# Kernel optimization log

Hardware: AMD Instinct MI355X
Metric: run time of the kernel (lower is better)

Reference implementation:

```python
import jax, jax.numpy as jnp
import numpy as np

N_QUBITS = 8
INPUT_DIM = 256
SEQ_LEN = 256
BATCH = 512


def qgate(theta, x):
    # Closed-form expectation of the PennyLane circuit:
    #   RX(x_i) then RY(theta_i) on each wire (from |0>), then CNOT chain 0->1->...->n-1,
    #   measure <Z_k>.  Single-wire <Z_j> = cos(x_j) * cos(theta_j); CNOT chain maps
    #   Z_k -> Z_0 Z_1 ... Z_k in the Heisenberg picture, so on the product state
    #   <Z_k> = prod_{j<=k} cos(x_j) cos(theta_j).
    # x: (B, n_wires), theta: (n_wires,)
    return jnp.cumprod(jnp.cos(x) * jnp.cos(theta), axis=-1)


def setup_inputs() -> dict:
    key = jax.random.key(0)
    ks = jax.random.split(key, 14)
    d_in = INPUT_DIM + N_QUBITS  # concat([x, hx]) -> 264
    lin_scale = 1.0 / np.sqrt(d_in)
    inp = {
        "inputs": jax.random.normal(ks[0], (SEQ_LEN, BATCH, INPUT_DIM), dtype=jnp.float32),
        "Wf": jax.random.normal(ks[1], (N_QUBITS, d_in), dtype=jnp.float32) * lin_scale,
        "bf": jax.random.normal(ks[2], (N_QUBITS,), dtype=jnp.float32) * lin_scale,
        "Wi": jax.random.normal(ks[3], (N_QUBITS, d_in), dtype=jnp.float32) * lin_scale,
        "bi": jax.random.normal(ks[4], (N_QUBITS,), dtype=jnp.float32) * lin_scale,
        "Wu": jax.random.normal(ks[5], (N_QUBITS, d_in), dtype=jnp.float32) * lin_scale,
        "bu": jax.random.normal(ks[6], (N_QUBITS,), dtype=jnp.float32) * lin_scale,
        "Wo": jax.random.normal(ks[7], (N_QUBITS, d_in), dtype=jnp.float32) * lin_scale,
        "bo": jax.random.normal(ks[8], (N_QUBITS,), dtype=jnp.float32) * lin_scale,
        "pf": jax.random.normal(ks[9], (N_QUBITS,), dtype=jnp.float32),
        "pi_": jax.random.normal(ks[10], (N_QUBITS,), dtype=jnp.float32),
        "pu": jax.random.normal(ks[11], (N_QUBITS,), dtype=jnp.float32),
        "po": jax.random.normal(ks[12], (N_QUBITS,), dtype=jnp.float32),
    }
    return inp


def reference(inputs, Wf, bf, Wi, bi, Wu, bu, Wo, bo, pf, pi_, pu, po):
    B = inputs.shape[1]
    H = pf.shape[0]  # hidden_dim == n_qubits

    def step(carry, x):
        hx, cx = carry
        comb = jnp.concatenate([x, hx], axis=1)  # (B, input_dim + H)
        f = jax.nn.sigmoid(qgate(pf, comb @ Wf.T + bf))
        i = jax.nn.sigmoid(qgate(pi_, comb @ Wi.T + bi))
        g = jnp.tanh(qgate(pu, comb @ Wu.T + bu))
        o = jax.nn.sigmoid(qgate(po, comb @ Wo.T + bo))
        cx = f * cx + i * g
        hx = o * jnp.tanh(cx)
        return (hx, cx), hx

    init = (jnp.zeros((B, H), dtype=inputs.dtype), jnp.zeros((B, H), dtype=inputs.dtype))
    (hx, cx), stacked = jax.lax.scan(step, init, inputs)
    return stacked, hx, cx
```

## Files before the change

### kernel.cpp

```cpp
#include <hip/hip_runtime.h>
#include <hip/hip_bf16.h>


#define SEQ   256
#define BATCH 512
#define DIN   256
#define NROWS (SEQ * BATCH)
#define DCOMB 264
#define MCHUNKS 4

typedef __attribute__((ext_vector_type(8))) short short8;
typedef __attribute__((ext_vector_type(4))) float f32x4;
typedef __attribute__((ext_vector_type(2))) float f32x2;

__device__ __forceinline__ short f2bf(float f) {
    union { __hip_bfloat16 h; short s; } u;
    u.h = __float2bfloat16(f);
    return u.s;
}
__device__ __forceinline__ float bf2f(short s) {
    union { short s; __hip_bfloat16 h; } u;
    u.s = s;
    return __bfloat162float(u.h);
}

__device__ __forceinline__ short8 pack8(float4 a, float4 b) {
    union { short8 s8; int i[4]; } u;
    union { __hip_bfloat162 h; int i; } v;
    v.h = __float22bfloat162_rn(make_float2(a.x, a.y)); u.i[0] = v.i;
    v.h = __float22bfloat162_rn(make_float2(a.z, a.w)); u.i[1] = v.i;
    v.h = __float22bfloat162_rn(make_float2(b.x, b.y)); u.i[2] = v.i;
    v.h = __float22bfloat162_rn(make_float2(b.z, b.w)); u.i[3] = v.i;
    return u.s8;
}

__global__ __launch_bounds__(256) void qlstm_gemm(
    const float* __restrict__ X,
    const float* __restrict__ Wf, const float* __restrict__ Wi,
    const float* __restrict__ Wu, const float* __restrict__ Wo,
    const float* __restrict__ bfv, const float* __restrict__ biv,
    const float* __restrict__ buv, const float* __restrict__ bov,
    float* __restrict__ Z)
{
    const int l   = threadIdx.x & 63;
    const int wid = threadIdx.x >> 6;
    const int lm  = l & 15;
    const int lk  = l >> 4;

    const float* Wg[4] = {Wf, Wi, Wu, Wo};
    const float* Bg[4] = {bfv, biv, buv, bov};

    short8 Bhi[2][8], Blo[2][8];
    float bias[2];
    #pragma unroll
    for (int nt = 0; nt < 2; ++nt) {
        const int c = nt * 16 + lm;
        const float* wrow = Wg[c & 3] + (c >> 2) * DCOMB;
        bias[nt] = Bg[c & 3][c >> 2];
        #pragma unroll
        for (int ks = 0; ks < 8; ++ks) {
            const float* p = wrow + ks * 32 + lk * 8;
            const float4 w0 = *(const float4*)p;
            const float4 w1 = *(const float4*)(p + 4);
            const float wv[8] = {w0.x, w0.y, w0.z, w0.w, w1.x, w1.y, w1.z, w1.w};
            #pragma unroll
            for (int j = 0; j < 8; ++j) {
                const short hi = f2bf(wv[j]);
                Bhi[nt][ks][j] = hi;
                Blo[nt][ks][j] = f2bf(wv[j] - bf2f(hi));
            }
        }
    }

    #pragma unroll
    for (int ch = 0; ch < MCHUNKS; ++ch) {
        const int row0 = (blockIdx.x * MCHUNKS + ch) * 64 + wid * 16;
        const float* xbase = X + (long)(row0 + lm) * DIN + lk * 8;

        float4 xv[16];
        #pragma unroll
        for (int i = 0; i < 16; ++i)
            xv[i] = *(const float4*)(xbase + (i >> 1) * 32 + (i & 1) * 4);

        f32x4 acc0 = (f32x4){bias[0], bias[0], bias[0], bias[0]};
        f32x4 acc1 = (f32x4){bias[1], bias[1], bias[1], bias[1]};
        #pragma unroll
        for (int ks = 0; ks < 8; ++ks) {
            const short8 a = pack8(xv[2 * ks], xv[2 * ks + 1]);
            acc0 = __builtin_amdgcn_mfma_f32_16x16x32_bf16(a, Bhi[0][ks], acc0, 0, 0, 0);
            acc0 = __builtin_amdgcn_mfma_f32_16x16x32_bf16(a, Blo[0][ks], acc0, 0, 0, 0);
            acc1 = __builtin_amdgcn_mfma_f32_16x16x32_bf16(a, Bhi[1][ks], acc1, 0, 0, 0);
            acc1 = __builtin_amdgcn_mfma_f32_16x16x32_bf16(a, Blo[1][ks], acc1, 0, 0, 0);
        }

        #pragma unroll
        for (int r = 0; r < 4; ++r) {
            Z[(long)(row0 + lk * 4 + r) * 32 + lm]      = acc0[r];
            Z[(long)(row0 + lk * 4 + r) * 32 + 16 + lm] = acc1[r];
        }
    }
}

#define DPP_ROR(V, S) \
    __int_as_float(__builtin_amdgcn_update_dpp(__float_as_int(V), __float_as_int(V), 0x120 | (S), 0xF, 0xF, false))
#define SWAP8(V) \
    __int_as_float(__builtin_amdgcn_update_dpp(__float_as_int(V), __float_as_int(V), 0x128, 0xF, 0xF, false))
#define DPP_REPL8(V) \
    __int_as_float(__builtin_amdgcn_update_dpp(__float_as_int(V), __float_as_int(V), 0x118, 0xF, 0xF, false))

#define PSTG(A, D, PM) { \
    float s0_ = __int_as_float(__builtin_amdgcn_update_dpp(one_i, __float_as_int(A.x), 0x110 | (D), 0xF, 0xF, false)); \
    float s1_ = __int_as_float(__builtin_amdgcn_update_dpp(one_i, __float_as_int(A.y), 0x110 | (D), 0xF, 0xF, false)); \
    A *= (f32x2){ (PM) ? s0_ : 1.0f, (PM) ? s1_ : 1.0f }; }

#define PF 8

__global__ __launch_bounds__(64, 1) void qlstm_scan(
    const float* __restrict__ Z,
    const float* __restrict__ Wf, const float* __restrict__ Wi,
    const float* __restrict__ Wu, const float* __restrict__ Wo,
    const float* __restrict__ pf, const float* __restrict__ pi_,
    const float* __restrict__ pu, const float* __restrict__ po,
    float* __restrict__ out)
{
    const int tx  = threadIdx.x;
    const int q   = tx & 15;
    const int kq  = q & 7;
    const int hi  = q >> 3;
    const int b   = (blockIdx.x * 64 + tx) >> 4;
    const int oidx = b * 8 + kq;
    const int woff = kq * DCOMB + DIN;

    const float* WgA = hi ? Wu : Wf;
    const float* WgB = hi ? Wo : Wi;
    f32x2 wp[8];
    #pragma unroll
    for (int s = 0; s < 8; ++s) {
        const int j = (kq - s) & 7;
        wp[s] = (f32x2){WgA[woff + j], WgB[woff + j]};
    }
    const f32x2 cth = (f32x2){__cosf((hi ? pu : pf)[kq]),
                              __cosf((hi ? po : pi_)[kq])};

    const float SK1 = 0.25f, SK2 = -0.0208333333f, SK3 = 0.0020833333f,
                SK4 = -0.00021082f;
    const f32x2 k0 = (f32x2){hi ? 0.0f : 0.5f, 0.5f};
    const f32x2 k1 = (f32x2){hi ? 0.9999016f : SK1, SK1};
    const f32x2 k2 = (f32x2){hi ? -0.3310485f : SK2, SK2};
    const f32x2 k3 = (f32x2){hi ? 0.1204423f : SK3, SK3};
    const f32x2 k4 = (f32x2){hi ? -0.0277012f : SK4, SK4};

    const bool pm1 = kq >= 1, pm2 = kq >= 2, pm4 = kq >= 4;
    const int one_i = __float_as_int(1.0f);

    float hx = 0.0f, cx = 0.0f;
    const float2* __restrict__ Zv2 = (const float2*)Z;
    const int zoff = b * 16 + kq * 2 + hi;
    float* __restrict__ outp = out + oidx;

    float2 ring[PF];
    #pragma unroll
    for (int i = 0; i < PF; ++i) ring[i] = Zv2[(i << 13) + zoff];

    for (int t0 = 0; t0 < SEQ; t0 += PF) {
        #pragma unroll
        for (int u = 0; u < PF; ++u) {
            const int t = t0 + u;
            const float2 z2 = ring[u];
            int tn = t + PF; if (tn > SEQ - 1) tn = SEQ - 1;
            ring[u] = Zv2[(tn << 13) + zoff];

            const float h0 = hx;
            const float h1 = DPP_ROR(hx, 1), h2 = DPP_ROR(hx, 2);
            const float h3 = DPP_ROR(hx, 3), h4 = DPP_ROR(hx, 4);
            const float h5 = DPP_ROR(hx, 5), h6 = DPP_ROR(hx, 6);
            const float h7 = DPP_ROR(hx, 7);

            f32x2 ca = (f32x2){h0, h0} * wp[0] + (f32x2){h1, h1} * wp[1];
            f32x2 cb = (f32x2){h4, h4} * wp[4] + (f32x2){h5, h5} * wp[5];
            ca += (f32x2){h2, h2} * wp[2];
            cb += (f32x2){h6, h6} * wp[6];
            ca += (f32x2){h3, h3} * wp[3];
            cb += (f32x2){h7, h7} * wp[7];
            const f32x2 p = ((f32x2){z2.x, z2.y} + ca) + cb;

            f32x2 A = (f32x2){__cosf(p.x), __cosf(p.y)} * cth;
            PSTG(A, 1, pm1) PSTG(A, 2, pm2) PSTG(A, 4, pm4)

            const f32x2 t2 = A * A;
            f32x2 r = k3 + t2 * k4;
            r = k2 + t2 * r;
            r = k1 + t2 * r;
            const f32x2 P = k0 + A * r;
            const float v1 = P.x;
            const float v2 = P.y;

            const float swu = SWAP8(v1);
            cx = fmaf(v1, cx, v2 * swu);

            const float tq  = cx * cx;
            const float num = cx * fmaf(tq, fmaf(tq, 1.0f, 105.0f), 945.0f);
            const float den = fmaf(tq, fmaf(tq, 15.0f, 420.0f), 945.0f);
            const float tc  = num * __builtin_amdgcn_rcpf(den);

            const float stc = SWAP8(tc);
            const float hh  = v2 * stc;
            hx = SWAP8(hh);
            hx = DPP_REPL8(hx);

            outp[t << 12] = hx;
        }
    }
    if (q < 8) {
        out[NROWS * 8 + oidx]        = hx;
        out[NROWS * 8 + 4096 + oidx] = cx;
    }
}

extern "C" void kernel_launch(void* const* d_in, const int* in_sizes, int n_in,
                              void* d_out, int out_size, void* d_ws, size_t ws_size,
                              hipStream_t stream) {
    const float* X   = (const float*)d_in[0];
    const float* Wf  = (const float*)d_in[1];
    const float* bfv = (const float*)d_in[2];
    const float* Wi  = (const float*)d_in[3];
    const float* biv = (const float*)d_in[4];
    const float* Wu  = (const float*)d_in[5];
    const float* buv = (const float*)d_in[6];
    const float* Wo  = (const float*)d_in[7];
    const float* bov = (const float*)d_in[8];
    const float* pf  = (const float*)d_in[9];
    const float* pi_ = (const float*)d_in[10];
    const float* pu  = (const float*)d_in[11];
    const float* po  = (const float*)d_in[12];
    float* out = (float*)d_out;
    float* Z   = (float*)d_ws;

    qlstm_gemm<<<NROWS / (64 * MCHUNKS), 256, 0, stream>>>(
        X, Wf, Wi, Wu, Wo, bfv, biv, buv, bov, Z);
    qlstm_scan<<<128, 64, 0, stream>>>(Z, Wf, Wi, Wu, Wo, pf, pi_, pu, po, out);
}
```

Measured before the change: 264.8 us.

## Fuse projection GEMM and recurrent scan with flag-based producer-consumer overlap

```diff
diff --git a/kernel.cpp b/kernel.cpp
--- a/kernel.cpp
+++ b/kernel.cpp
@@ -7,7 +7,13 @@
 #define DIN   256
 #define NROWS (SEQ * BATCH)
 #define DCOMB 264
-#define MCHUNKS 4
+#define ZBYTES (NROWS * 32 * 4)
+
+#define NSCAN  32
+#define NBLK   512
+#define WSLOTS ((NBLK - NSCAN) * 4)
+#define NCHUNK (NROWS / 16)
+#define MAGIC  0x13579BDFu
 
 typedef __attribute__((ext_vector_type(8))) short short8;
 typedef __attribute__((ext_vector_type(4))) float f32x4;
@@ -23,7 +29,6 @@
     u.s = s;
     return __bfloat162float(u.h);
 }
-
 __device__ __forceinline__ short8 pack8(float4 a, float4 b) {
     union { short8 s8; int i[4]; } u;
     union { __hip_bfloat162 h; int i; } v;
@@ -34,80 +39,12 @@
     return u.s8;
 }
 
-__global__ __launch_bounds__(256) void qlstm_gemm(
-    const float* __restrict__ X,
-    const float* __restrict__ Wf, const float* __restrict__ Wi,
-    const float* __restrict__ Wu, const float* __restrict__ Wo,
-    const float* __restrict__ bfv, const float* __restrict__ biv,
-    const float* __restrict__ buv, const float* __restrict__ bov,
-    float* __restrict__ Z)
-{
-    const int l   = threadIdx.x & 63;
-    const int wid = threadIdx.x >> 6;
-    const int lm  = l & 15;
-    const int lk  = l >> 4;
-
-    const float* Wg[4] = {Wf, Wi, Wu, Wo};
-    const float* Bg[4] = {bfv, biv, buv, bov};
-
-    short8 Bhi[2][8], Blo[2][8];
-    float bias[2];
-    #pragma unroll
-    for (int nt = 0; nt < 2; ++nt) {
-        const int c = nt * 16 + lm;
-        const float* wrow = Wg[c & 3] + (c >> 2) * DCOMB;
-        bias[nt] = Bg[c & 3][c >> 2];
-        #pragma unroll
-        for (int ks = 0; ks < 8; ++ks) {
-            const float* p = wrow + ks * 32 + lk * 8;
-            const float4 w0 = *(const float4*)p;
-            const float4 w1 = *(const float4*)(p + 4);
-            const float wv[8] = {w0.x, w0.y, w0.z, w0.w, w1.x, w1.y, w1.z, w1.w};
-            #pragma unroll
-            for (int j = 0; j < 8; ++j) {
-                const short hi = f2bf(wv[j]);
-                Bhi[nt][ks][j] = hi;
-                Blo[nt][ks][j] = f2bf(wv[j] - bf2f(hi));
-            }
-        }
-    }
-
-    #pragma unroll
-    for (int ch = 0; ch < MCHUNKS; ++ch) {
-        const int row0 = (blockIdx.x * MCHUNKS + ch) * 64 + wid * 16;
-        const float* xbase = X + (long)(row0 + lm) * DIN + lk * 8;
-
-        float4 xv[16];
-        #pragma unroll
-        for (int i = 0; i < 16; ++i)
-            xv[i] = *(const float4*)(xbase + (i >> 1) * 32 + (i & 1) * 4);
-
-        f32x4 acc0 = (f32x4){bias[0], bias[0], bias[0], bias[0]};
-        f32x4 acc1 = (f32x4){bias[1], bias[1], bias[1], bias[1]};
-        #pragma unroll
-        for (int ks = 0; ks < 8; ++ks) {
-            const short8 a = pack8(xv[2 * ks], xv[2 * ks + 1]);
-            acc0 = __builtin_amdgcn_mfma_f32_16x16x32_bf16(a, Bhi[0][ks], acc0, 0, 0, 0);
-            acc0 = __builtin_amdgcn_mfma_f32_16x16x32_bf16(a, Blo[0][ks], acc0, 0, 0, 0);
-            acc1 = __builtin_amdgcn_mfma_f32_16x16x32_bf16(a, Bhi[1][ks], acc1, 0, 0, 0);
-            acc1 = __builtin_amdgcn_mfma_f32_16x16x32_bf16(a, Blo[1][ks], acc1, 0, 0, 0);
-        }
-
-        #pragma unroll
-        for (int r = 0; r < 4; ++r) {
-            Z[(long)(row0 + lk * 4 + r) * 32 + lm]      = acc0[r];
-            Z[(long)(row0 + lk * 4 + r) * 32 + 16 + lm] = acc1[r];
-        }
-    }
-}
-
 #define DPP_ROR(V, S) \
     __int_as_float(__builtin_amdgcn_update_dpp(__float_as_int(V), __float_as_int(V), 0x120 | (S), 0xF, 0xF, false))
 #define SWAP8(V) \
     __int_as_float(__builtin_amdgcn_update_dpp(__float_as_int(V), __float_as_int(V), 0x128, 0xF, 0xF, false))
 #define DPP_REPL8(V) \
     __int_as_float(__builtin_amdgcn_update_dpp(__float_as_int(V), __float_as_int(V), 0x118, 0xF, 0xF, false))
-
 #define PSTG(A, D, PM) { \
     float s0_ = __int_as_float(__builtin_amdgcn_update_dpp(one_i, __float_as_int(A.x), 0x110 | (D), 0xF, 0xF, false)); \
     float s1_ = __int_as_float(__builtin_amdgcn_update_dpp(one_i, __float_as_int(A.y), 0x110 | (D), 0xF, 0xF, false)); \
@@ -115,19 +52,91 @@
 
 #define PF 8
 
-__global__ __launch_bounds__(64, 1) void qlstm_scan(
-    const float* __restrict__ Z,
+__global__ __launch_bounds__(256) void flags_zero(unsigned* __restrict__ flags) {
+    flags[blockIdx.x * 256 + threadIdx.x] = 0u;
+}
+
+__global__ __launch_bounds__(256, 2) void qlstm_fused(
+    const float* __restrict__ X,
     const float* __restrict__ Wf, const float* __restrict__ Wi,
     const float* __restrict__ Wu, const float* __restrict__ Wo,
+    const float* __restrict__ bfv, const float* __restrict__ biv,
+    const float* __restrict__ buv, const float* __restrict__ bov,
     const float* __restrict__ pf, const float* __restrict__ pi_,
     const float* __restrict__ pu, const float* __restrict__ po,
+    float* __restrict__ Z, unsigned* __restrict__ flags,
     float* __restrict__ out)
 {
-    const int tx  = threadIdx.x;
-    const int q   = tx & 15;
-    const int kq  = q & 7;
-    const int hi  = q >> 3;
-    const int b   = (blockIdx.x * 64 + tx) >> 4;
+    const int wid = threadIdx.x >> 6;
+    const int l   = threadIdx.x & 63;
+
+    if (blockIdx.x >= NSCAN) {
+        const int lm = l & 15, lk = l >> 4;
+        const float* Wg[4] = {Wf, Wi, Wu, Wo};
+        const float* Bg[4] = {bfv, biv, buv, bov};
+
+        short8 Bhi[2][8], Blo[2][8];
+        float bias[2];
+        #pragma unroll
+        for (int nt = 0; nt < 2; ++nt) {
+            const int c = nt * 16 + lm;
+            const float* wrow = Wg[c & 3] + (c >> 2) * DCOMB;
+            bias[nt] = Bg[c & 3][c >> 2];
+            #pragma unroll
+            for (int ks = 0; ks < 8; ++ks) {
+                const float* p = wrow + ks * 32 + lk * 8;
+                const float4 w0 = *(const float4*)p;
+                const float4 w1 = *(const float4*)(p + 4);
+                const float wv[8] = {w0.x, w0.y, w0.z, w0.w, w1.x, w1.y, w1.z, w1.w};
+                #pragma unroll
+                for (int j = 0; j < 8; ++j) {
+                    const short hi = f2bf(wv[j]);
+                    Bhi[nt][ks][j] = hi;
+                    Blo[nt][ks][j] = f2bf(wv[j] - bf2f(hi));
+                }
+            }
+        }
+
+        const int wslot = (blockIdx.x - NSCAN) * 4 + wid;
+        #pragma unroll 1
+        for (int c = wslot; c < NCHUNK; c += WSLOTS) {
+            const int row0 = c * 16;
+            const float* xbase = X + (long)(row0 + lm) * DIN + lk * 8;
+
+            float4 xv[16];
+            #pragma unroll
+            for (int i = 0; i < 16; ++i)
+                xv[i] = *(const float4*)(xbase + (i >> 1) * 32 + (i & 1) * 4);
+
+            f32x4 acc0 = (f32x4){bias[0], bias[0], bias[0], bias[0]};
+            f32x4 acc1 = (f32x4){bias[1], bias[1], bias[1], bias[1]};
+            #pragma unroll
+            for (int ks = 0; ks < 8; ++ks) {
+                const short8 a = pack8(xv[2 * ks], xv[2 * ks + 1]);
+                acc0 = __builtin_amdgcn_mfma_f32_16x16x32_bf16(a, Bhi[0][ks], acc0, 0, 0, 0);
+                acc0 = __builtin_amdgcn_mfma_f32_16x16x32_bf16(a, Blo[0][ks], acc0, 0, 0, 0);
+                acc1 = __builtin_amdgcn_mfma_f32_16x16x32_bf16(a, Bhi[1][ks], acc1, 0, 0, 0);
+                acc1 = __builtin_amdgcn_mfma_f32_16x16x32_bf16(a, Blo[1][ks], acc1, 0, 0, 0);
+            }
+
+            #pragma unroll
+            for (int r = 0; r < 4; ++r) {
+                Z[(long)(row0 + lk * 4 + r) * 32 + lm]      = acc0[r];
+                Z[(long)(row0 + lk * 4 + r) * 32 + 16 + lm] = acc1[r];
+            }
+
+            if (l == 0)
+                __hip_atomic_store(&flags[c], MAGIC, __ATOMIC_RELEASE,
+                                   __HIP_MEMORY_SCOPE_AGENT);
+        }
+        return;
+    }
+
+    const int sid  = blockIdx.x * 256 + threadIdx.x;
+    const int q    = sid & 15;
+    const int kq   = q & 7;
+    const int hi   = q >> 3;
+    const int b    = sid >> 4;
     const int oidx = b * 8 + kq;
     const int woff = kq * DCOMB + DIN;
 
@@ -154,21 +163,49 @@
     const int one_i = __float_as_int(1.0f);
 
     float hx = 0.0f, cx = 0.0f;
-    const float2* __restrict__ Zv2 = (const float2*)Z;
     const int zoff = b * 16 + kq * 2 + hi;
     float* __restrict__ outp = out + oidx;
 
+    #define LDF(S, J) __hip_atomic_load( \
+        flags + ((S) * 32) + (l * 4 + (J)), __ATOMIC_RELAXED, __HIP_MEMORY_SCOPE_AGENT)
+    #define ZLD(SL) ({ \
+        union { unsigned long long u; float2 f; } cv_; \
+        cv_.u = __hip_atomic_load((const unsigned long long*)Z + \
+                 (((long)(SL)) << 13) + zoff, __ATOMIC_RELAXED, \
+                 __HIP_MEMORY_SCOPE_AGENT); \
+        cv_.f; })
+
+    #define SPIN8(S0) { \
+        for (int sp_ = 0; sp_ < (1 << 17); ++sp_) { \
+            unsigned a_ = LDF(S0, 0), b_ = LDF(S0, 1); \
+            unsigned c_ = LDF(S0, 2), d_ = LDF(S0, 3); \
+            if (__all((a_ == MAGIC) & (b_ == MAGIC) & (c_ == MAGIC) & (d_ == MAGIC))) break; \
+            __builtin_amdgcn_s_sleep(8); \
+        } }
+
+    SPIN8(0)
     float2 ring[PF];
     #pragma unroll
-    for (int i = 0; i < PF; ++i) ring[i] = Zv2[(i << 13) + zoff];
-
+    for (int i = 0; i < PF; ++i) ring[i] = ZLD(i);
+    unsigned f0 = LDF(PF, 0), f1 = LDF(PF, 1);
+    unsigned f2 = LDF(PF, 2), f3 = LDF(PF, 3);
+
+    #pragma unroll 1
     for (int t0 = 0; t0 < SEQ; t0 += PF) {
+        if (t0 + PF < SEQ) {
+            if (!__all((f0 == MAGIC) & (f1 == MAGIC) & (f2 == MAGIC) & (f3 == MAGIC)))
+                SPIN8(t0 + PF)
+            if (t0 + 2 * PF < SEQ) {
+                f0 = LDF(t0 + 2 * PF, 0); f1 = LDF(t0 + 2 * PF, 1);
+                f2 = LDF(t0 + 2 * PF, 2); f3 = LDF(t0 + 2 * PF, 3);
+            }
+        }
         #pragma unroll
         for (int u = 0; u < PF; ++u) {
             const int t = t0 + u;
             const float2 z2 = ring[u];
             int tn = t + PF; if (tn > SEQ - 1) tn = SEQ - 1;
-            ring[u] = Zv2[(tn << 13) + zoff];
+            ring[u] = ZLD(tn);
 
             const float h0 = hx;
             const float h1 = DPP_ROR(hx, 1), h2 = DPP_ROR(hx, 2);
@@ -234,9 +271,12 @@
     const float* pu  = (const float*)d_in[11];
     const float* po  = (const float*)d_in[12];
     float* out = (float*)d_out;
-    float* Z   = (float*)d_ws;
-
-    qlstm_gemm<<<NROWS / (64 * MCHUNKS), 256, 0, stream>>>(
-        X, Wf, Wi, Wu, Wo, bfv, biv, buv, bov, Z);
-    qlstm_scan<<<128, 64, 0, stream>>>(Z, Wf, Wi, Wu, Wo, pf, pi_, pu, po, out);
-}
+
+    char* ws = (char*)d_ws;
+    float*    Z     = (float*)ws;
+    unsigned* flags = (unsigned*)(ws + ZBYTES);
+
+    flags_zero<<<NCHUNK / 256, 256, 0, stream>>>(flags);
+    qlstm_fused<<<NBLK, 256, 0, stream>>>(
+        X, Wf, Wi, Wu, Wo, bfv, biv, buv, bov, pf, pi_, pu, po, Z, flags, out);
+}
```

Measured after the change: 512.1 us. 1.93x slower.
